# Kernel optimization log

Measured on AMD Instinct MI355X. Metric: run time of the kernel, lower is better.

Reference implementation:

```python
import math
import jax, jax.numpy as jnp
import numpy as np

B, L, D = 8, 4096, 512
FACTOR = 5


def setup_inputs() -> dict:
    key = jax.random.key(0)
    kq, kk, kv = jax.random.split(key, 3)
    q = jax.random.normal(kq, (B, L, D), dtype=jnp.float32)
    k = jax.random.normal(kk, (B, L, D), dtype=jnp.float32)
    v = jax.random.normal(kv, (B, L, D), dtype=jnp.float32)
    return {"q": q, "k": k, "v": v}


def reference(q, k, v):
    # ProbSparse attention (sparse=True branch, L_Q > 1)
    L_Q = q.shape[1]
    scale = q.shape[-1] ** -0.5
    # scores: [B, L_Q, L_K]
    scores = jnp.einsum('bqd,bkd->bqk', q, k) * scale
    # sparsity measure M = max - mean over keys: [B, L_Q]
    M = scores.max(axis=-1) - scores.mean(axis=-1)
    u = max(1, int(FACTOR * math.log(L_Q + 1)))
    u = min(u, L_Q)  # static python int (u = 41 here)
    _, top_idx = jax.lax.top_k(M, u)  # [B, u]
    # gather top-u query rows of scores, softmax over keys (row-wise softmax
    # commutes with row selection, so this matches softmax-then-gather)
    scores_top = jnp.take_along_axis(scores, top_idx[:, :, None], axis=1)  # [B, u, L_K]
    attn = jax.nn.softmax(scores_top, axis=-1)
    out_top = jnp.einsum('buk,bkd->bud', attn, v)  # [B, u, D]
    # non-selected queries receive the mean value
    v_mean = jnp.broadcast_to(v.mean(axis=1, keepdims=True), v.shape)  # [B, L, D]
    b_idx = jnp.arange(q.shape[0])[:, None]  # [B, 1]
    out = v_mean.at[b_idx, top_idx].set(out_top)
    return out
```

## Files before the change

### kernel.cpp

```cpp
#include <hip/hip_runtime.h>
#include <math.h>

#define B_ 8
#define L_ 4096
#define D_ 512
#define U_ 41
#define NSL 32

static constexpr float SCALE = 0.044194173824159216f;

typedef __attribute__((ext_vector_type(8))) short bf16x8;
typedef __attribute__((ext_vector_type(4))) float f32x4;
typedef unsigned int uint;


__global__ __launch_bounds__(512) void kSumsV4(const float* __restrict__ k,
                                               const float* __restrict__ v,
                                               float* __restrict__ partk,
                                               float* __restrict__ partv) {
  const int s = blockIdx.x;
  const int b = blockIdx.y;
  const int rg = threadIdx.x >> 7;
  const int dc = threadIdx.x & 127;
  const int row0 = s * 128 + rg * 32;
  const float* kp = k + ((size_t)(b * L_ + row0)) * D_ + dc * 4;
  const float* vp = v + ((size_t)(b * L_ + row0)) * D_ + dc * 4;
  float4 ks = make_float4(0.f, 0.f, 0.f, 0.f);
  float4 vs = make_float4(0.f, 0.f, 0.f, 0.f);
  for (int l = 0; l < 32; ++l) {
    float4 t = *(const float4*)(kp + (size_t)l * D_);
    float4 u = *(const float4*)(vp + (size_t)l * D_);
    ks.x += t.x; ks.y += t.y; ks.z += t.z; ks.w += t.w;
    vs.x += u.x; vs.y += u.y; vs.z += u.z; vs.w += u.w;
  }
  const int p = (b * NSL + s) * 4 + rg;
  *(float4*)(partk + (size_t)p * D_ + dc * 4) = ks;
  *(float4*)(partv + (size_t)p * D_ + dc * 4) = vs;
}

__global__ __launch_bounds__(512) void kSums2V(const float* __restrict__ partk,
                                               const float* __restrict__ partv,
                                               float* __restrict__ ksum,
                                               float* __restrict__ vmean) {
  const int b = blockIdx.x;
  const int d = threadIdx.x;
  float ks = 0.f, vs = 0.f;
  for (int p = 0; p < 128; ++p) {
    ks += partk[((size_t)(b * 128 + p)) * D_ + d];
    vs += partv[((size_t)(b * 128 + p)) * D_ + d];
  }
  ksum[b * D_ + d] = ks;
  vmean[b * D_ + d] = vs * (1.f / L_);
}

__global__ __launch_bounds__(512) void kSums1(const float* __restrict__ k,
                                              const float* __restrict__ v,
                                              float* __restrict__ partk,
                                              float* __restrict__ partv) {
  const int s = blockIdx.x;
  const int b = blockIdx.y;
  const int d = threadIdx.x;
  const int rows = L_ / NSL;
  const size_t base = ((size_t)b * L_ + (size_t)s * rows) * D_ + d;
  float ks = 0.f, vs = 0.f;
  for (int l = 0; l < rows; ++l) {
    ks += k[base + (size_t)l * D_];
    vs += v[base + (size_t)l * D_];
  }
  partk[(b * NSL + s) * D_ + d] = ks;
  partv[(b * NSL + s) * D_ + d] = vs;
}

__global__ __launch_bounds__(512) void kSums2(const float* __restrict__ partk,
                                              const float* __restrict__ partv,
                                              float* __restrict__ ksum,
                                              float* __restrict__ vmean) {
  const int b = blockIdx.x;
  const int d = threadIdx.x;
  float ks = 0.f, vs = 0.f;
  for (int s = 0; s < NSL; ++s) {
    ks += partk[(b * NSL + s) * D_ + d];
    vs += partv[(b * NSL + s) * D_ + d];
  }
  ksum[b * D_ + d] = ks;
  vmean[b * D_ + d] = vs * (1.f / L_);
}

__global__ __launch_bounds__(256) void kMeanM(const float* __restrict__ q,
                                              const float* __restrict__ ksum,
                                              const float* __restrict__ pmax,
                                              float* __restrict__ M) {
  __shared__ float ks[D_];
  const int gid = blockIdx.x * 256 + threadIdx.x;
  const int b = gid >> 12;
  for (int i = threadIdx.x; i < D_; i += 256) ks[i] = ksum[b * D_ + i];
  __syncthreads();
  const float* qp = q + (size_t)gid * D_;
  float acc = 0.f;
  for (int i = 0; i < D_; i += 4) {
    float4 t = *(const float4*)(qp + i);
    acc += t.x * ks[i] + t.y * ks[i + 1] + t.z * ks[i + 2] + t.w * ks[i + 3];
  }
  const float rowmax = fmaxf(pmax[gid], pmax[B_ * L_ + gid]);
  M[gid] = SCALE * (rowmax - acc * (1.f / L_));
}

__global__ __launch_bounds__(256) void kTopK3(const float* __restrict__ M,
                                              int* __restrict__ topidx) {
  __shared__ float wv[2][4];
  __shared__ int wi[2][4];
  const int b = blockIdx.x;
  const int tid = threadIdx.x;
  const int wave = tid >> 6, lane = tid & 63;
  float v[16];
#pragma unroll
  for (int j = 0; j < 16; ++j) v[j] = M[b * L_ + tid + j * 256];
  float bv = v[0];
  int bj = 0;
#pragma unroll
  for (int j = 1; j < 16; ++j)
    if (v[j] > bv) { bv = v[j]; bj = j; }
  int bi = tid + bj * 256;

  for (int it = 0; it < U_; ++it) {
    float rv = bv;
    int ri = bi;
#pragma unroll
    for (int off = 1; off < 64; off <<= 1) {
      float ov = __shfl_xor(rv, off);
      int oi = __shfl_xor(ri, off);
      if (ov > rv || (ov == rv && oi < ri)) { rv = ov; ri = oi; }
    }
    const int par = it & 1;
    if (lane == 0) { wv[par][wave] = rv; wi[par][wave] = ri; }
    __syncthreads();
    float gv = wv[par][0];
    int gi = wi[par][0];
#pragma unroll
    for (int w = 1; w < 4; ++w) {
      float ov = wv[par][w];
      int oi = wi[par][w];
      if (ov > gv || (ov == gv && oi < gi)) { gv = ov; gi = oi; }
    }
    if (tid == 0) topidx[b * U_ + it] = gi;
    if (gi == bi) {
      const int jb = gi >> 8;
#pragma unroll
      for (int j = 0; j < 16; ++j)
        if (j == jb) v[j] = -3.4e38f;
      bv = v[0];
      bj = 0;
#pragma unroll
      for (int j = 1; j < 16; ++j)
        if (v[j] > bv) { bv = v[j]; bj = j; }
      bi = tid + bj * 256;
    }
  }
}

__global__ __launch_bounds__(64) void kTopK4(const float* __restrict__ pmax,
                                             const float* __restrict__ qdot,
                                             int* __restrict__ topidx) {
  const int b = blockIdx.x;
  const int lane = threadIdx.x;
  float v[64];
#pragma unroll
  for (int j = 0; j < 64; ++j) {
    const int gid = b * L_ + lane + j * 64;
    v[j] = SCALE * (fmaxf(pmax[gid], pmax[B_ * L_ + gid]) - qdot[gid] * (1.f / L_));
  }
  float bv = v[0];
  int bj = 0;
#pragma unroll
  for (int j = 1; j < 64; ++j)
    if (v[j] > bv) { bv = v[j]; bj = j; }
  int bi = lane + bj * 64;

  for (int it = 0; it < U_; ++it) {
    float rv = bv;
    int ri = bi;
#pragma unroll
    for (int off = 1; off < 64; off <<= 1) {
      float ov = __shfl_xor(rv, off);
      int oi = __shfl_xor(ri, off);
      if (ov > rv || (ov == rv && oi < ri)) { rv = ov; ri = oi; }
    }
    if (lane == 0) topidx[b * U_ + it] = ri;
    if (ri == bi) {
#pragma unroll
      for (int j = 0; j < 64; ++j)
        if (j == bj) v[j] = -3.4e38f;
      bv = v[0];
      bj = 0;
#pragma unroll
      for (int j = 1; j < 64; ++j)
        if (v[j] > bv) { bv = v[j]; bj = j; }
      bi = lane + bj * 64;
    }
  }
}

__global__ __launch_bounds__(256) void kFill(const float* __restrict__ vmean,
                                             float* __restrict__ out) {
  const int g = blockIdx.x * 256 + threadIdx.x;
  const int d4 = g & 127;
  const int bl = g >> 7;
  const int b = bl >> 12;
  ((float4*)out)[g] = ((const float4*)vmean)[b * 128 + d4];
}

__device__ inline uint bf16_rne_bits(float x) {
  uint u = __builtin_bit_cast(uint, x);
  return (u + 0x7FFFu + ((u >> 16) & 1u)) >> 16;
}
__device__ inline float bits_to_f32(uint hi16) {
  return __builtin_bit_cast(float, hi16 << 16);
}

__global__ __launch_bounds__(256) void kConvert(const float* __restrict__ src,
                                                unsigned char* __restrict__ dhi,
                                                unsigned char* __restrict__ dlo) {
  const int cid = blockIdx.x * 256 + threadIdx.x;
  const int c16 = cid & 7;
  const int row = (cid >> 3) & 127;
  const int dsi = (cid >> 10) & 7;
  const int rt = (cid >> 13) & 31;
  const int b = cid >> 18;
  const int l = rt * 128 + row;
  const int d = dsi * 64 + c16 * 8;
  const float* sp = src + ((size_t)(b * L_ + l) * D_ + d);
  float x[8];
  *(float4*)(x) = *(const float4*)sp;
  *(float4*)(x + 4) = *(const float4*)(sp + 4);
  uint hw[4], lw[4];
#pragma unroll
  for (int p = 0; p < 4; ++p) {
    float a = x[2 * p], c = x[2 * p + 1];
    uint ha = bf16_rne_bits(a), hc = bf16_rne_bits(c);
    float ra = a - bits_to_f32(ha);
    float rc = c - bits_to_f32(hc);
    uint la = bf16_rne_bits(ra), lc = bf16_rne_bits(rc);
    hw[p] = ha | (hc << 16);
    lw[p] = la | (lc << 16);
  }
  const size_t dstByte = ((size_t)(cid >> 3) << 7) +
                         (uint)((c16 << 4) ^ ((row & 7) << 4));
  *(uint4*)(dhi + dstByte) = make_uint4(hw[0], hw[1], hw[2], hw[3]);
  *(uint4*)(dlo + dstByte) = make_uint4(lw[0], lw[1], lw[2], lw[3]);
}

__global__ __launch_bounds__(256) void kConvertQdot(const float* __restrict__ src,
                                                    const float* __restrict__ ksum,
                                                    unsigned char* __restrict__ dhi,
                                                    unsigned char* __restrict__ dlo,
                                                    float* __restrict__ qdotp) {
  const int cid = blockIdx.x * 256 + threadIdx.x;
  const int c16 = cid & 7;
  const int row = (cid >> 3) & 127;
  const int dsi = (cid >> 10) & 7;
  const int rt = (cid >> 13) & 31;
  const int b = cid >> 18;
  const int l = rt * 128 + row;
  const int d = dsi * 64 + c16 * 8;
  const float* sp = src + ((size_t)(b * L_ + l) * D_ + d);
  float x[8];
  *(float4*)(x) = *(const float4*)sp;
  *(float4*)(x + 4) = *(const float4*)(sp + 4);

  const float* kp = ksum + b * D_ + d;
  float dot = 0.f;
#pragma unroll
  for (int i = 0; i < 8; ++i) dot += x[i] * kp[i];
#pragma unroll
  for (int off = 1; off < 8; off <<= 1) dot += __shfl_xor(dot, off);

  uint hw[4], lw[4];
#pragma unroll
  for (int p = 0; p < 4; ++p) {
    float a = x[2 * p], c = x[2 * p + 1];
    uint ha = bf16_rne_bits(a), hc = bf16_rne_bits(c);
    float ra = a - bits_to_f32(ha);
    float rc = c - bits_to_f32(hc);
    uint la = bf16_rne_bits(ra), lc = bf16_rne_bits(rc);
    hw[p] = ha | (hc << 16);
    lw[p] = la | (lc << 16);
  }
  const size_t dstByte = ((size_t)(cid >> 3) << 7) +
                         (uint)((c16 << 4) ^ ((row & 7) << 4));
  *(uint4*)(dhi + dstByte) = make_uint4(hw[0], hw[1], hw[2], hw[3]);
  *(uint4*)(dlo + dstByte) = make_uint4(lw[0], lw[1], lw[2], lw[3]);
  if (c16 == 0)
    qdotp[((size_t)dsi * B_ * L_) + b * L_ + l] = dot;
}

__global__ __launch_bounds__(256) void kQdotReduce(const float* __restrict__ qdotp,
                                                   float* __restrict__ qdot) {
  const int gid = blockIdx.x * 256 + threadIdx.x;
  float s = 0.f;
#pragma unroll
  for (int i = 0; i < 8; ++i) s += qdotp[(size_t)i * B_ * L_ + gid];
  qdot[gid] = s;
}

__device__ __forceinline__ void gload16(const unsigned char* g, unsigned char* l) {
  __builtin_amdgcn_global_load_lds(
      (const __attribute__((address_space(1))) unsigned int*)(g),
      (__attribute__((address_space(3))) unsigned int*)(l), 16, 0, 0);
}

__global__ __launch_bounds__(256, 2) void kRowMaxB(const unsigned char* __restrict__ qhi,
                                                   const unsigned char* __restrict__ qlo,
                                                   const unsigned char* __restrict__ khi,
                                                   const unsigned char* __restrict__ klo,
                                                   float* __restrict__ pmax) {
  __shared__ unsigned char lds[65536];
  __shared__ float red[256];
  unsigned char* ldsQhi = lds;
  unsigned char* ldsQlo = lds + 16384;
  unsigned char* ldsKhi = lds + 32768;
  unsigned char* ldsKlo = lds + 49152;

  const int b = blockIdx.y;
  const int qt = blockIdx.x;
  const int kh = blockIdx.z;
  const int tid = threadIdx.x;
  const int lane = tid & 63;
  const int wave = tid >> 6;
  const int wq = wave >> 1, wk = wave & 1;

  const size_t qtb = ((size_t)((b * 32 + qt) * 8)) * 16384;
  const unsigned char* qhB = qhi + qtb;
  const unsigned char* qlB = qlo + qtb;

  float rmax[4][4];
#pragma unroll
  for (int i = 0; i < 4; ++i)
#pragma unroll
    for (int j = 0; j < 4; ++j) rmax[i][j] = -3.4e38f;

  for (int kt = 0; kt < 16; ++kt) {
    const size_t ktb = ((size_t)((b * 32 + (kh * 16 + kt)) * 8)) * 16384;
    const unsigned char* khB = khi + ktb;
    const unsigned char* klB = klo + ktb;

    f32x4 acc[4][4];
#pragma unroll
    for (int i = 0; i < 4; ++i)
#pragma unroll
      for (int j = 0; j < 4; ++j)
#pragma unroll
        for (int e = 0; e < 4; ++e) acc[i][j][e] = 0.f;

    for (int dsi = 0; dsi < 8; ++dsi) {
      __syncthreads();
      {
        const size_t dof = (size_t)dsi * 16384 + (size_t)tid * 16;
        const size_t lof = (size_t)tid * 16;
#pragma unroll
        for (int i = 0; i < 4; ++i) {
          gload16(qhB + dof + i * 4096, ldsQhi + lof + i * 4096);
          gload16(qlB + dof + i * 4096, ldsQlo + lof + i * 4096);
          gload16(khB + dof + i * 4096, ldsKhi + lof + i * 4096);
          gload16(klB + dof + i * 4096, ldsKlo + lof + i * 4096);
        }
      }
      __syncthreads();

#pragma unroll
      for (int h = 0; h < 2; ++h) {
        const int rbyte = h * 64 + ((lane >> 4) << 4);
        bf16x8 aH[4], aL[4], bH[4], bL[4];
#pragma unroll
        for (int f = 0; f < 4; ++f) {
          const int qrow = wq * 64 + f * 16 + (lane & 15);
          const int krow = wk * 64 + f * 16 + (lane & 15);
          const int qoff = qrow * 128 + (rbyte ^ ((qrow & 7) << 4));
          const int koff = krow * 128 + (rbyte ^ ((krow & 7) << 4));
          aH[f] = *(const bf16x8*)(ldsQhi + qoff);
          aL[f] = *(const bf16x8*)(ldsQlo + qoff);
          bH[f] = *(const bf16x8*)(ldsKhi + koff);
          bL[f] = *(const bf16x8*)(ldsKlo + koff);
        }
#pragma unroll
        for (int mf = 0; mf < 4; ++mf)
#pragma unroll
          for (int nf = 0; nf < 4; ++nf) {
            acc[mf][nf] = __builtin_amdgcn_mfma_f32_16x16x32_bf16(aH[mf], bH[nf], acc[mf][nf], 0, 0, 0);
            acc[mf][nf] = __builtin_amdgcn_mfma_f32_16x16x32_bf16(aH[mf], bL[nf], acc[mf][nf], 0, 0, 0);
            acc[mf][nf] = __builtin_amdgcn_mfma_f32_16x16x32_bf16(aL[mf], bH[nf], acc[mf][nf], 0, 0, 0);
          }
      }
    }
#pragma unroll
    for (int mf = 0; mf < 4; ++mf)
#pragma unroll
      for (int r = 0; r < 4; ++r) {
        float m = fmaxf(fmaxf(acc[mf][0][r], acc[mf][1][r]),
                        fmaxf(acc[mf][2][r], acc[mf][3][r]));
        rmax[mf][r] = fmaxf(rmax[mf][r], m);
      }
  }

#pragma unroll
  for (int mf = 0; mf < 4; ++mf)
#pragma unroll
    for (int r = 0; r < 4; ++r) {
      float v = rmax[mf][r];
#pragma unroll
      for (int off = 1; off < 16; off <<= 1) v = fmaxf(v, __shfl_xor(v, off));
      rmax[mf][r] = v;
    }

  if ((lane & 15) == 0) {
#pragma unroll
    for (int mf = 0; mf < 4; ++mf)
#pragma unroll
      for (int r = 0; r < 4; ++r) {
        const int rowl = wq * 64 + mf * 16 + ((lane >> 4) << 2) + r;
        red[wk * 128 + rowl] = rmax[mf][r];
      }
  }
  __syncthreads();
  if (tid < 128) {
    pmax[(size_t)kh * B_ * L_ + (size_t)b * L_ + qt * 128 + tid] =
        fmaxf(red[tid], red[128 + tid]);
  }
}


__global__ __launch_bounds__(64) void kGatherQ(const float* __restrict__ q,
                                               const int* __restrict__ topidx,
                                               unsigned char* __restrict__ qselhi,
                                               unsigned char* __restrict__ qsello) {
  const int j = blockIdx.x;
  const int b = blockIdx.y;
  const int lane = threadIdx.x;
  const int dsi = lane >> 3;
  const int c16 = lane & 7;
  float x[8] = {0.f, 0.f, 0.f, 0.f, 0.f, 0.f, 0.f, 0.f};
  if (j < U_) {
    const int row = topidx[b * U_ + j];
    const float* sp = q + ((size_t)(b * L_ + row)) * D_ + dsi * 64 + c16 * 8;
    *(float4*)(x) = *(const float4*)sp;
    *(float4*)(x + 4) = *(const float4*)(sp + 4);
  }
  uint hw[4], lw[4];
#pragma unroll
  for (int p = 0; p < 4; ++p) {
    float a = x[2 * p], c = x[2 * p + 1];
    uint ha = bf16_rne_bits(a), hc = bf16_rne_bits(c);
    float ra = a - bits_to_f32(ha);
    float rc = c - bits_to_f32(hc);
    uint la = bf16_rne_bits(ra), lc = bf16_rne_bits(rc);
    hw[p] = ha | (hc << 16);
    lw[p] = la | (lc << 16);
  }
  const size_t dstByte = ((size_t)((b * 8 + dsi) * 64 + j)) * 128 +
                         (uint)((c16 << 4) ^ ((j & 7) << 4));
  *(uint4*)(qselhi + dstByte) = make_uint4(hw[0], hw[1], hw[2], hw[3]);
  *(uint4*)(qsello + dstByte) = make_uint4(lw[0], lw[1], lw[2], lw[3]);
}

__global__ __launch_bounds__(256) void kSelScoresM(const unsigned char* __restrict__ qselhi,
                                                   const unsigned char* __restrict__ qsello,
                                                   const unsigned char* __restrict__ khi,
                                                   const unsigned char* __restrict__ klo,
                                                   float* __restrict__ P) {
  __shared__ unsigned char lds[49152];
  unsigned char* ldsQhi = lds;
  unsigned char* ldsQlo = lds + 8192;
  unsigned char* ldsKhi = lds + 16384;
  unsigned char* ldsKlo = lds + 32768;

  const int kc = blockIdx.x;
  const int b = blockIdx.y;
  const int tid = threadIdx.x;
  const int lane = tid & 63;
  const int wave = tid >> 6;
  const int wq = wave >> 1, wk = wave & 1;

  const size_t ktb = ((size_t)((b * 32 + kc) * 8)) * 16384;
  const unsigned char* khB = khi + ktb;
  const unsigned char* klB = klo + ktb;
  const size_t qb = ((size_t)b * 8) * 8192;
  const unsigned char* qhB = qselhi + qb;
  const unsigned char* qlB = qsello + qb;

  f32x4 acc[2][4];
#pragma unroll
  for (int i = 0; i < 2; ++i)
#pragma unroll
    for (int j = 0; j < 4; ++j)
#pragma unroll
      for (int e = 0; e < 4; ++e) acc[i][j][e] = 0.f;

  for (int dsi = 0; dsi < 8; ++dsi) {
    __syncthreads();
    {
      const size_t qof = (size_t)dsi * 8192 + (size_t)tid * 16;
      const size_t kof = (size_t)dsi * 16384 + (size_t)tid * 16;
      const size_t lof = (size_t)tid * 16;
#pragma unroll
      for (int i = 0; i < 2; ++i) {
        gload16(qhB + qof + i * 4096, ldsQhi + lof + i * 4096);
        gload16(qlB + qof + i * 4096, ldsQlo + lof + i * 4096);
      }
#pragma unroll
      for (int i = 0; i < 4; ++i) {
        gload16(khB + kof + i * 4096, ldsKhi + lof + i * 4096);
        gload16(klB + kof + i * 4096, ldsKlo + lof + i * 4096);
      }
    }
    __syncthreads();

#pragma unroll
    for (int h = 0; h < 2; ++h) {
      const int rbyte = h * 64 + ((lane >> 4) << 4);
      bf16x8 aH[2], aL[2], bH[4], bL[4];
#pragma unroll
      for (int f = 0; f < 2; ++f) {
        const int qrow = wq * 32 + f * 16 + (lane & 15);
        const int qoff = qrow * 128 + (rbyte ^ ((qrow & 7) << 4));
        aH[f] = *(const bf16x8*)(ldsQhi + qoff);
        aL[f] = *(const bf16x8*)(ldsQlo + qoff);
      }
#pragma unroll
      for (int f = 0; f < 4; ++f) {
        const int krow = wk * 64 + f * 16 + (lane & 15);
        const int koff = krow * 128 + (rbyte ^ ((krow & 7) << 4));
        bH[f] = *(const bf16x8*)(ldsKhi + koff);
        bL[f] = *(const bf16x8*)(ldsKlo + koff);
      }
#pragma unroll
      for (int mf = 0; mf < 2; ++mf)
#pragma unroll
        for (int nf = 0; nf < 4; ++nf) {
          acc[mf][nf] = __builtin_amdgcn_mfma_f32_16x16x32_bf16(aH[mf], bH[nf], acc[mf][nf], 0, 0, 0);
          acc[mf][nf] = __builtin_amdgcn_mfma_f32_16x16x32_bf16(aH[mf], bL[nf], acc[mf][nf], 0, 0, 0);
          acc[mf][nf] = __builtin_amdgcn_mfma_f32_16x16x32_bf16(aL[mf], bH[nf], acc[mf][nf], 0, 0, 0);
        }
    }
  }

#pragma unroll
  for (int mf = 0; mf < 2; ++mf)
#pragma unroll
    for (int nf = 0; nf < 4; ++nf)
#pragma unroll
      for (int r = 0; r < 4; ++r) {
        const int row = wq * 32 + mf * 16 + ((lane >> 4) << 2) + r;
        const int key = kc * 128 + wk * 64 + nf * 16 + (lane & 15);
        if (row < U_)
          P[((size_t)(b * U_ + row)) * L_ + key] = acc[mf][nf][r];
      }
}

__global__ __launch_bounds__(256) void kSoftmaxP(float* __restrict__ P) {
  __shared__ float red[256];
  const int j = blockIdx.x, b = blockIdx.y;
  float* row = P + ((size_t)(b * U_ + j)) * L_;
  const int tid = threadIdx.x;
  float v[16];
  float mx = -3.4e38f;
#pragma unroll
  for (int i = 0; i < 16; ++i) {
    v[i] = row[tid + i * 256];
    mx = fmaxf(mx, v[i]);
  }
  red[tid] = mx;
  __syncthreads();
  for (int s = 128; s > 0; s >>= 1) {
    if (tid < s) red[tid] = fmaxf(red[tid], red[tid + s]);
    __syncthreads();
  }
  mx = red[0];
  __syncthreads();
  float sum = 0.f;
#pragma unroll
  for (int i = 0; i < 16; ++i) {
    float e = expf((v[i] - mx) * SCALE);
    v[i] = e;
    sum += e;
  }
  red[tid] = sum;
  __syncthreads();
  for (int s = 128; s > 0; s >>= 1) {
    if (tid < s) red[tid] += red[tid + s];
    __syncthreads();
  }
  const float inv = 1.f / red[0];
#pragma unroll
  for (int i = 0; i < 16; ++i) row[tid + i * 256] = v[i] * inv;
}

__global__ __launch_bounds__(256) void kPV(const float* __restrict__ P,
                                           const float* __restrict__ v,
                                           float* __restrict__ partial) {
  __shared__ float plds[41 * 128];
  const int kc = blockIdx.x;
  const int dc = blockIdx.y;
  const int b = blockIdx.z;
  const int tid = threadIdx.x;
  const int trow = tid >> 7, dcol = tid & 127;
  float acc[U_];
#pragma unroll
  for (int j = 0; j < U_; ++j) acc[j] = 0.f;

  for (int sub = 0; sub < 4; ++sub) {
    const int key0 = kc * 512 + sub * 128;
    __syncthreads();
    for (int idx = tid; idx < U_ * 128; idx += 256)
      plds[idx] = P[((size_t)(b * U_ + (idx >> 7))) * L_ + key0 + (idx & 127)];
    __syncthreads();
    const float* vp = v + ((size_t)(b * L_ + key0 + trow * 64)) * D_ + dc * 128 + dcol;
    float vv[64];
#pragma unroll
    for (int kk = 0; kk < 64; ++kk) vv[kk] = vp[(size_t)kk * D_];
#pragma unroll
    for (int j = 0; j < U_; ++j) {
      const float4* pr = (const float4*)&plds[j * 128 + trow * 64];
      float a = acc[j];
#pragma unroll
      for (int q4 = 0; q4 < 16; ++q4) {
        float4 p4 = pr[q4];
        a = fmaf(p4.x, vv[q4 * 4 + 0], a);
        a = fmaf(p4.y, vv[q4 * 4 + 1], a);
        a = fmaf(p4.z, vv[q4 * 4 + 2], a);
        a = fmaf(p4.w, vv[q4 * 4 + 3], a);
      }
      acc[j] = a;
    }
  }
  float* pp = partial + ((size_t)((b * 4 + dc) * 16 + kc * 2 + trow)) * (U_ * 128) + dcol;
#pragma unroll
  for (int j = 0; j < U_; ++j) pp[j * 128] = acc[j];
}

__global__ __launch_bounds__(256) void kPVout(const float* __restrict__ partial,
                                              const int* __restrict__ topidx,
                                              float* __restrict__ out) {
  const int j = blockIdx.x, b = blockIdx.y;
  const int tid = threadIdx.x;
  const int l = topidx[b * U_ + j];
#pragma unroll
  for (int h = 0; h < 2; ++h) {
    const int d = tid + h * 256;
    const int dc = d >> 7, dcol = d & 127;
    float s = 0.f;
#pragma unroll
    for (int part = 0; part < 16; ++part)
      s += partial[((size_t)((b * 4 + dc) * 16 + part)) * (U_ * 128) + j * 128 + dcol];
    out[((size_t)(b * L_ + l)) * D_ + d] = s;
  }
}


__device__ inline void stageHalfRow(const float* __restrict__ src,
                                    char* hiBase, char* loBase,
                                    int row, int shalf) {
  const int sw = (row & 7) << 4;
  char* hp = hiBase + row * 128;
  char* lp = loBase + row * 128;
#pragma unroll
  for (int g = 0; g < 4; ++g) {
    f32x4 x0 = *(const f32x4*)(src + g * 8);
    f32x4 x1 = *(const f32x4*)(src + g * 8 + 4);
    float x[8] = {x0.x, x0.y, x0.z, x0.w, x1.x, x1.y, x1.z, x1.w};
    uint hw[4], lw[4];
#pragma unroll
    for (int p = 0; p < 4; ++p) {
      float a = x[2 * p], c = x[2 * p + 1];
      uint ha = bf16_rne_bits(a), hc = bf16_rne_bits(c);
      float ra = a - bits_to_f32(ha);
      float rc = c - bits_to_f32(hc);
      uint la = bf16_rne_bits(ra), lc = bf16_rne_bits(rc);
      hw[p] = ha | (hc << 16);
      lw[p] = la | (lc << 16);
    }
    const int off = (shalf * 64 + g * 16) ^ sw;
    *(uint4*)(hp + off) = make_uint4(hw[0], hw[1], hw[2], hw[3]);
    *(uint4*)(lp + off) = make_uint4(lw[0], lw[1], lw[2], lw[3]);
  }
}

__global__ __launch_bounds__(256, 2) void kRowMaxM(const float* __restrict__ q,
                                                   const float* __restrict__ k,
                                                   float* __restrict__ pmax) {
  __shared__ char lds[65536];
  __shared__ float red[256];
  char* ldsQhi = lds;
  char* ldsQlo = lds + 16384;
  char* ldsKhi = lds + 32768;
  char* ldsKlo = lds + 49152;

  const int b = blockIdx.y;
  const int qbase = blockIdx.x * 128;
  const int kh = blockIdx.z;
  const int tid = threadIdx.x;
  const int lane = tid & 63;
  const int wave = tid >> 6;
  const int wq = wave >> 1, wk = wave & 1;
  const int srow = tid >> 1;
  const int shalf = tid & 1;

  const float* qrow_base = q + ((size_t)b * L_ + qbase + srow) * D_ + shalf * 32;
  const float* krow_base = k + ((size_t)b * L_ + kh * 2048 + srow) * D_ + shalf * 32;

  float rmax[4][4];
#pragma unroll
  for (int i = 0; i < 4; ++i)
#pragma unroll
    for (int j = 0; j < 4; ++j) rmax[i][j] = -3.4e38f;

  for (int kt = 0; kt < 16; ++kt) {
    f32x4 acc[4][4];
#pragma unroll
    for (int i = 0; i < 4; ++i)
#pragma unroll
      for (int j = 0; j < 4; ++j)
#pragma unroll
        for (int e = 0; e < 4; ++e) acc[i][j][e] = 0.f;

    for (int dsi = 0; dsi < 8; ++dsi) {
      __syncthreads();
      stageHalfRow(qrow_base + dsi * 64, ldsQhi, ldsQlo, srow, shalf);
      stageHalfRow(krow_base + (size_t)kt * 128 * D_ + dsi * 64, ldsKhi, ldsKlo, srow, shalf);
      __syncthreads();

#pragma unroll
      for (int h = 0; h < 2; ++h) {
        const int rbyte = h * 64 + ((lane >> 4) << 4);
        bf16x8 aH[4], aL[4], bH[4], bL[4];
#pragma unroll
        for (int f = 0; f < 4; ++f) {
          const int qrow = wq * 64 + f * 16 + (lane & 15);
          const int krow = wk * 64 + f * 16 + (lane & 15);
          const int qoff = qrow * 128 + (rbyte ^ ((qrow & 7) << 4));
          const int koff = krow * 128 + (rbyte ^ ((krow & 7) << 4));
          aH[f] = *(const bf16x8*)(ldsQhi + qoff);
          aL[f] = *(const bf16x8*)(ldsQlo + qoff);
          bH[f] = *(const bf16x8*)(ldsKhi + koff);
          bL[f] = *(const bf16x8*)(ldsKlo + koff);
        }
#pragma unroll
        for (int mf = 0; mf < 4; ++mf)
#pragma unroll
          for (int nf = 0; nf < 4; ++nf) {
            acc[mf][nf] = __builtin_amdgcn_mfma_f32_16x16x32_bf16(aH[mf], bH[nf], acc[mf][nf], 0, 0, 0);
            acc[mf][nf] = __builtin_amdgcn_mfma_f32_16x16x32_bf16(aH[mf], bL[nf], acc[mf][nf], 0, 0, 0);
            acc[mf][nf] = __builtin_amdgcn_mfma_f32_16x16x32_bf16(aL[mf], bH[nf], acc[mf][nf], 0, 0, 0);
          }
      }
    }
#pragma unroll
    for (int mf = 0; mf < 4; ++mf)
#pragma unroll
      for (int r = 0; r < 4; ++r) {
        float m = fmaxf(fmaxf(acc[mf][0][r], acc[mf][1][r]),
                        fmaxf(acc[mf][2][r], acc[mf][3][r]));
        rmax[mf][r] = fmaxf(rmax[mf][r], m);
      }
  }

#pragma unroll
  for (int mf = 0; mf < 4; ++mf)
#pragma unroll
    for (int r = 0; r < 4; ++r) {
      float v = rmax[mf][r];
#pragma unroll
      for (int off = 1; off < 16; off <<= 1) v = fmaxf(v, __shfl_xor(v, off));
      rmax[mf][r] = v;
    }

  if ((lane & 15) == 0) {
#pragma unroll
    for (int mf = 0; mf < 4; ++mf)
#pragma unroll
      for (int r = 0; r < 4; ++r) {
        const int rowl = wq * 64 + mf * 16 + ((lane >> 4) << 2) + r;
        red[wk * 128 + rowl] = rmax[mf][r];
      }
  }
  __syncthreads();
  if (tid < 128) {
    pmax[(size_t)kh * B_ * L_ + (size_t)b * L_ + qbase + tid] =
        fmaxf(red[tid], red[128 + tid]);
  }
}

__global__ __launch_bounds__(256) void kAttnSel(const float* __restrict__ q,
                                                const float* __restrict__ k,
                                                const float* __restrict__ v,
                                                const int* __restrict__ topidx,
                                                float* __restrict__ out) {
  __shared__ float qs[D_];
  __shared__ float sc[L_];
  __shared__ float wred[4];
  __shared__ float sred[256];
  const int b = blockIdx.y;
  const int l_sel = topidx[b * U_ + blockIdx.x];
  const int tid = threadIdx.x;
  const int wave = tid >> 6, lane = tid & 63;
  const float* qrow = q + ((size_t)b * L_ + l_sel) * D_;
  qs[tid] = qrow[tid];
  qs[tid + 256] = qrow[tid + 256];
  __syncthreads();
  float qr[8];
#pragma unroll
  for (int i = 0; i < 8; ++i) qr[i] = qs[lane * 8 + i];
  float wmax = -3.4e38f;
  for (int l = wave; l < L_; l += 4) {
    const float* kp = k + ((size_t)b * L_ + l) * D_ + lane * 8;
    float4 k0 = *(const float4*)kp;
    float4 k1 = *(const float4*)(kp + 4);
    float p = k0.x * qr[0] + k0.y * qr[1] + k0.z * qr[2] + k0.w * qr[3] +
              k1.x * qr[4] + k1.y * qr[5] + k1.z * qr[6] + k1.w * qr[7];
#pragma unroll
    for (int off = 32; off > 0; off >>= 1) p += __shfl_xor(p, off);
    if (lane == 0) sc[l] = p;
    wmax = fmaxf(wmax, p);
  }
  if (lane == 0) wred[wave] = wmax;
  __syncthreads();
  const float mx = fmaxf(fmaxf(wred[0], wred[1]), fmaxf(wred[2], wred[3]));
  float psum = 0.f;
  for (int i = tid; i < L_; i += 256) {
    float e = expf((sc[i] - mx) * SCALE);
    sc[i] = e;
    psum += e;
  }
  sred[tid] = psum;
  __syncthreads();
  for (int s = 128; s > 0; s >>= 1) {
    if (tid < s) sred[tid] += sred[tid + s];
    __syncthreads();
  }
  const float inv = 1.f / sred[0];
  float a0a = 0.f, a0b = 0.f, a1a = 0.f, a1b = 0.f;
  const float* vb = v + (size_t)b * L_ * D_;
  for (int l = 0; l < L_; l += 2) {
    float p0 = sc[l], p1 = sc[l + 1];
    const float* vp0 = vb + (size_t)l * D_;
    const float* vp1 = vp0 + D_;
    a0a = fmaf(p0, vp0[tid], a0a);
    a1a = fmaf(p0, vp0[tid + 256], a1a);
    a0b = fmaf(p1, vp1[tid], a0b);
    a1b = fmaf(p1, vp1[tid + 256], a1b);
  }
  float* orow = out + ((size_t)b * L_ + l_sel) * D_;
  orow[tid] = (a0a + a0b) * inv;
  orow[tid + 256] = (a1a + a1b) * inv;
}


extern "C" void kernel_launch(void* const* d_in, const int* in_sizes, int n_in,
                              void* d_out, int out_size, void* d_ws, size_t ws_size,
                              hipStream_t stream) {
  const float* q = (const float*)d_in[0];
  const float* k = (const float*)d_in[1];
  const float* v = (const float*)d_in[2];
  float* out = (float*)d_out;
  unsigned char* wsb = (unsigned char*)d_ws;

  const size_t NEED = 71731200;

  if (ws_size >= NEED) {
    unsigned char* qhiW = wsb;
    unsigned char* qloW = wsb + 33554432;
    float* P = (float*)wsb;
    float* partial = (float*)(wsb + 5373952);
    unsigned char* qselhi = wsb + 16121856;
    unsigned char* qsello = wsb + 16646144;
    float* pmax = (float*)(wsb + 67108864);
    float* qdot = (float*)(wsb + 67371008);
    float* ksum = (float*)(wsb + 67502080);
    float* vmean = (float*)(wsb + 67518464);
    int* tidx = (int*)(wsb + 67534848);
    float* partk = (float*)(wsb + 67536896);
    float* partv = (float*)(wsb + 69634048);
    float* qdotp = partk;

    unsigned char* khiO = (unsigned char*)d_out;
    unsigned char* kloO = khiO + 33554432;

    kSumsV4<<<dim3(NSL, B_), 512, 0, stream>>>(k, v, partk, partv);
    kSums2V<<<B_, 512, 0, stream>>>(partk, partv, ksum, vmean);
    kConvertQdot<<<8192, 256, 0, stream>>>(q, ksum, qhiW, qloW, qdotp);
    kQdotReduce<<<B_ * L_ / 256, 256, 0, stream>>>(qdotp, qdot);
    kConvert<<<8192, 256, 0, stream>>>(k, khiO, kloO);
    kRowMaxB<<<dim3(32, B_, 2), 256, 0, stream>>>(qhiW, qloW, khiO, kloO, pmax);
    kTopK4<<<B_, 64, 0, stream>>>(pmax, qdot, tidx);
    kGatherQ<<<dim3(64, B_), 64, 0, stream>>>(q, tidx, qselhi, qsello);
    kSelScoresM<<<dim3(32, B_), 256, 0, stream>>>(qselhi, qsello, khiO, kloO, P);
    kSoftmaxP<<<dim3(U_, B_), 256, 0, stream>>>(P);
    kFill<<<B_ * L_ * D_ / 1024, 256, 0, stream>>>(vmean, out);
    kPV<<<dim3(8, 4, B_), 256, 0, stream>>>(P, v, partial);
    kPVout<<<dim3(U_, B_), 256, 0, stream>>>(partial, tidx, out);
  } else {
    float* ws = (float*)d_ws;
    float* Marr = ws;
    float* pmax = ws + 32768;
    float* ksum = ws + 98304;
    float* vmean = ws + 102400;
    int* tidx = (int*)(ws + 106496);
    float* partk = ws + 107008;
    float* partv = ws + 107008 + B_ * NSL * D_;

    kSums1<<<dim3(NSL, B_), 512, 0, stream>>>(k, v, partk, partv);
    kSums2<<<B_, 512, 0, stream>>>(partk, partv, ksum, vmean);
    kRowMaxM<<<dim3(L_ / 128, B_, 2), 256, 0, stream>>>(q, k, pmax);
    kMeanM<<<B_ * L_ / 256, 256, 0, stream>>>(q, ksum, pmax, Marr);
    kTopK3<<<B_, 256, 0, stream>>>(Marr, tidx);
    kFill<<<B_ * L_ * D_ / 1024, 256, 0, stream>>>(vmean, out);
    kAttnSel<<<dim3(U_, B_), 256, 0, stream>>>(q, k, v, tidx, out);
  }
}
```

Before: 601.3 us.

## Double-buffer row-max GEMM with 32-wide d-slices and flattened k-loop

The bf16 hi/lo split layout goes from 64-column to 32-column d-slices with a matching 4-chunk XOR swizzle. The converter, gather and selected-scores kernels, and the qdot reduce (now 16 partials), are all updated to the new layout. The row-max kernel now runs one flattened loop over 256 stages with two 32 KB LDS buffers. The next stage's global-to-LDS loads are issued before the current stage's MFMAs, hiding load latency and dropping one barrier per step, at the cost of smaller per-stage MFMA work.

```diff
diff --git a/kernel.cpp b/kernel.cpp
--- a/kernel.cpp
+++ b/kernel.cpp
@@ -221,13 +221,13 @@
                                                 unsigned char* __restrict__ dhi,
                                                 unsigned char* __restrict__ dlo) {
   const int cid = blockIdx.x * 256 + threadIdx.x;
-  const int c16 = cid & 7;
-  const int row = (cid >> 3) & 127;
-  const int dsi = (cid >> 10) & 7;
+  const int c = cid & 3;
+  const int row = (cid >> 2) & 127;
+  const int dsi = (cid >> 9) & 15;
   const int rt = (cid >> 13) & 31;
   const int b = cid >> 18;
   const int l = rt * 128 + row;
-  const int d = dsi * 64 + c16 * 8;
+  const int d = dsi * 32 + c * 8;
   const float* sp = src + ((size_t)(b * L_ + l) * D_ + d);
   float x[8];
   *(float4*)(x) = *(const float4*)sp;
@@ -235,16 +235,16 @@
   uint hw[4], lw[4];
 #pragma unroll
   for (int p = 0; p < 4; ++p) {
-    float a = x[2 * p], c = x[2 * p + 1];
-    uint ha = bf16_rne_bits(a), hc = bf16_rne_bits(c);
+    float a = x[2 * p], cc = x[2 * p + 1];
+    uint ha = bf16_rne_bits(a), hc = bf16_rne_bits(cc);
     float ra = a - bits_to_f32(ha);
-    float rc = c - bits_to_f32(hc);
+    float rc = cc - bits_to_f32(hc);
     uint la = bf16_rne_bits(ra), lc = bf16_rne_bits(rc);
     hw[p] = ha | (hc << 16);
     lw[p] = la | (lc << 16);
   }
-  const size_t dstByte = ((size_t)(cid >> 3) << 7) +
-                         (uint)((c16 << 4) ^ ((row & 7) << 4));
+  const size_t dstByte = ((size_t)(cid >> 2) << 6) +
+                         (uint)((c ^ ((row >> 1) & 3)) << 4);
   *(uint4*)(dhi + dstByte) = make_uint4(hw[0], hw[1], hw[2], hw[3]);
   *(uint4*)(dlo + dstByte) = make_uint4(lw[0], lw[1], lw[2], lw[3]);
 }
@@ -255,13 +255,13 @@
                                                     unsigned char* __restrict__ dlo,
                                                     float* __restrict__ qdotp) {
   const int cid = blockIdx.x * 256 + threadIdx.x;
-  const int c16 = cid & 7;
-  const int row = (cid >> 3) & 127;
-  const int dsi = (cid >> 10) & 7;
+  const int c = cid & 3;
+  const int row = (cid >> 2) & 127;
+  const int dsi = (cid >> 9) & 15;
   const int rt = (cid >> 13) & 31;
   const int b = cid >> 18;
   const int l = rt * 128 + row;
-  const int d = dsi * 64 + c16 * 8;
+  const int d = dsi * 32 + c * 8;
   const float* sp = src + ((size_t)(b * L_ + l) * D_ + d);
   float x[8];
   *(float4*)(x) = *(const float4*)sp;
@@ -271,25 +271,25 @@
   float dot = 0.f;
 #pragma unroll
   for (int i = 0; i < 8; ++i) dot += x[i] * kp[i];
-#pragma unroll
-  for (int off = 1; off < 8; off <<= 1) dot += __shfl_xor(dot, off);
+  dot += __shfl_xor(dot, 1);
+  dot += __shfl_xor(dot, 2);
 
   uint hw[4], lw[4];
 #pragma unroll
   for (int p = 0; p < 4; ++p) {
-    float a = x[2 * p], c = x[2 * p + 1];
-    uint ha = bf16_rne_bits(a), hc = bf16_rne_bits(c);
+    float a = x[2 * p], cc = x[2 * p + 1];
+    uint ha = bf16_rne_bits(a), hc = bf16_rne_bits(cc);
     float ra = a - bits_to_f32(ha);
-    float rc = c - bits_to_f32(hc);
+    float rc = cc - bits_to_f32(hc);
     uint la = bf16_rne_bits(ra), lc = bf16_rne_bits(rc);
     hw[p] = ha | (hc << 16);
     lw[p] = la | (lc << 16);
   }
-  const size_t dstByte = ((size_t)(cid >> 3) << 7) +
-                         (uint)((c16 << 4) ^ ((row & 7) << 4));
+  const size_t dstByte = ((size_t)(cid >> 2) << 6) +
+                         (uint)((c ^ ((row >> 1) & 3)) << 4);
   *(uint4*)(dhi + dstByte) = make_uint4(hw[0], hw[1], hw[2], hw[3]);
   *(uint4*)(dlo + dstByte) = make_uint4(lw[0], lw[1], lw[2], lw[3]);
-  if (c16 == 0)
+  if (c == 0)
     qdotp[((size_t)dsi * B_ * L_) + b * L_ + l] = dot;
 }
 
@@ -298,7 +298,7 @@
   const int gid = blockIdx.x * 256 + threadIdx.x;
   float s = 0.f;
 #pragma unroll
-  for (int i = 0; i < 8; ++i) s += qdotp[(size_t)i * B_ * L_ + gid];
+  for (int i = 0; i < 16; ++i) s += qdotp[(size_t)i * B_ * L_ + gid];
   qdot[gid] = s;
 }
 
@@ -308,17 +308,15 @@
       (__attribute__((address_space(3))) unsigned int*)(l), 16, 0, 0);
 }
 
-__global__ __launch_bounds__(256, 2) void kRowMaxB(const unsigned char* __restrict__ qhi,
+__global__ __launch_bounds__(256, 2) void kRowMaxD(const unsigned char* __restrict__ qhi,
                                                    const unsigned char* __restrict__ qlo,
                                                    const unsigned char* __restrict__ khi,
                                                    const unsigned char* __restrict__ klo,
                                                    float* __restrict__ pmax) {
   __shared__ unsigned char lds[65536];
   __shared__ float red[256];
-  unsigned char* ldsQhi = lds;
-  unsigned char* ldsQlo = lds + 16384;
-  unsigned char* ldsKhi = lds + 32768;
-  unsigned char* ldsKlo = lds + 49152;
+  unsigned char* buf0 = lds;
+  unsigned char* buf1 = lds + 32768;
 
   const int b = blockIdx.y;
   const int qt = blockIdx.x;
@@ -327,78 +325,86 @@
   const int lane = tid & 63;
   const int wave = tid >> 6;
   const int wq = wave >> 1, wk = wave & 1;
-
-  const size_t qtb = ((size_t)((b * 32 + qt) * 8)) * 16384;
-  const unsigned char* qhB = qhi + qtb;
-  const unsigned char* qlB = qlo + qtb;
+  const int g4 = lane >> 4;
+
+  const unsigned char* qhB = qhi + (size_t)(b * 32 + qt) * 131072;
+  const unsigned char* qlB = qlo + (size_t)(b * 32 + qt) * 131072;
+  const unsigned char* khB = khi + (size_t)(b * 32 + kh * 16) * 131072;
+  const unsigned char* klB = klo + (size_t)(b * 32 + kh * 16) * 131072;
+
+  const size_t lof = (size_t)tid * 16;
+
+  auto STAGE = [&](int s, unsigned char* buf) {
+    const int kt = s >> 4, dsi = s & 15;
+    const size_t qof = (size_t)dsi * 8192 + lof;
+    const size_t kof = (size_t)kt * 131072 + (size_t)dsi * 8192 + lof;
+    gload16(qhB + qof, buf + lof);
+    gload16(qhB + qof + 4096, buf + lof + 4096);
+    gload16(qlB + qof, buf + 8192 + lof);
+    gload16(qlB + qof + 4096, buf + 8192 + lof + 4096);
+    gload16(khB + kof, buf + 16384 + lof);
+    gload16(khB + kof + 4096, buf + 16384 + lof + 4096);
+    gload16(klB + kof, buf + 24576 + lof);
+    gload16(klB + kof + 4096, buf + 24576 + lof + 4096);
+  };
 
   float rmax[4][4];
+  f32x4 acc[4][4];
 #pragma unroll
   for (int i = 0; i < 4; ++i)
 #pragma unroll
-    for (int j = 0; j < 4; ++j) rmax[i][j] = -3.4e38f;
-
-  for (int kt = 0; kt < 16; ++kt) {
-    const size_t ktb = ((size_t)((b * 32 + (kh * 16 + kt)) * 8)) * 16384;
-    const unsigned char* khB = khi + ktb;
-    const unsigned char* klB = klo + ktb;
-
-    f32x4 acc[4][4];
-#pragma unroll
-    for (int i = 0; i < 4; ++i)
-#pragma unroll
-      for (int j = 0; j < 4; ++j)
-#pragma unroll
-        for (int e = 0; e < 4; ++e) acc[i][j][e] = 0.f;
-
-    for (int dsi = 0; dsi < 8; ++dsi) {
-      __syncthreads();
-      {
-        const size_t dof = (size_t)dsi * 16384 + (size_t)tid * 16;
-        const size_t lof = (size_t)tid * 16;
-#pragma unroll
-        for (int i = 0; i < 4; ++i) {
-          gload16(qhB + dof + i * 4096, ldsQhi + lof + i * 4096);
-          gload16(qlB + dof + i * 4096, ldsQlo + lof + i * 4096);
-          gload16(khB + dof + i * 4096, ldsKhi + lof + i * 4096);
-          gload16(klB + dof + i * 4096, ldsKlo + lof + i * 4096);
+    for (int j = 0; j < 4; ++j) {
+      rmax[i][j] = -3.4e38f;
+#pragma unroll
+      for (int e = 0; e < 4; ++e) acc[i][j][e] = 0.f;
+    }
+
+  int qaddr[4], kaddr[4];
+#pragma unroll
+  for (int f = 0; f < 4; ++f) {
+    const int qrow = wq * 64 + f * 16 + (lane & 15);
+    const int krow = wk * 64 + f * 16 + (lane & 15);
+    qaddr[f] = qrow * 64 + ((g4 ^ ((qrow >> 1) & 3)) << 4);
+    kaddr[f] = krow * 64 + ((g4 ^ ((krow >> 1) & 3)) << 4);
+  }
+
+  auto PHASE = [&](int s, const unsigned char* bufR, unsigned char* bufW) {
+    __syncthreads();
+    if (s < 255) STAGE(s + 1, bufW);
+    bf16x8 aH[4], aL[4], bH[4], bL[4];
+#pragma unroll
+    for (int f = 0; f < 4; ++f) {
+      aH[f] = *(const bf16x8*)(bufR + qaddr[f]);
+      aL[f] = *(const bf16x8*)(bufR + 8192 + qaddr[f]);
+      bH[f] = *(const bf16x8*)(bufR + 16384 + kaddr[f]);
+      bL[f] = *(const bf16x8*)(bufR + 24576 + kaddr[f]);
+    }
+#pragma unroll
+    for (int mf = 0; mf < 4; ++mf)
+#pragma unroll
+      for (int nf = 0; nf < 4; ++nf) {
+        acc[mf][nf] = __builtin_amdgcn_mfma_f32_16x16x32_bf16(aH[mf], bH[nf], acc[mf][nf], 0, 0, 0);
+        acc[mf][nf] = __builtin_amdgcn_mfma_f32_16x16x32_bf16(aH[mf], bL[nf], acc[mf][nf], 0, 0, 0);
+        acc[mf][nf] = __builtin_amdgcn_mfma_f32_16x16x32_bf16(aL[mf], bH[nf], acc[mf][nf], 0, 0, 0);
+      }
+    if ((s & 15) == 15) {
+#pragma unroll
+      for (int mf = 0; mf < 4; ++mf)
+#pragma unroll
+        for (int r = 0; r < 4; ++r) {
+          float m = fmaxf(fmaxf(acc[mf][0][r], acc[mf][1][r]),
+                          fmaxf(acc[mf][2][r], acc[mf][3][r]));
+          rmax[mf][r] = fmaxf(rmax[mf][r], m);
+#pragma unroll
+          for (int nf = 0; nf < 4; ++nf) acc[mf][nf][r] = 0.f;
         }
-      }
-      __syncthreads();
-
-#pragma unroll
-      for (int h = 0; h < 2; ++h) {
-        const int rbyte = h * 64 + ((lane >> 4) << 4);
-        bf16x8 aH[4], aL[4], bH[4], bL[4];
-#pragma unroll
-        for (int f = 0; f < 4; ++f) {
-          const int qrow = wq * 64 + f * 16 + (lane & 15);
-          const int krow = wk * 64 + f * 16 + (lane & 15);
-          const int qoff = qrow * 128 + (rbyte ^ ((qrow & 7) << 4));
-          const int koff = krow * 128 + (rbyte ^ ((krow & 7) << 4));
-          aH[f] = *(const bf16x8*)(ldsQhi + qoff);
-          aL[f] = *(const bf16x8*)(ldsQlo + qoff);
-          bH[f] = *(const bf16x8*)(ldsKhi + koff);
-          bL[f] = *(const bf16x8*)(ldsKlo + koff);
-        }
-#pragma unroll
-        for (int mf = 0; mf < 4; ++mf)
-#pragma unroll
-          for (int nf = 0; nf < 4; ++nf) {
-            acc[mf][nf] = __builtin_amdgcn_mfma_f32_16x16x32_bf16(aH[mf], bH[nf], acc[mf][nf], 0, 0, 0);
-            acc[mf][nf] = __builtin_amdgcn_mfma_f32_16x16x32_bf16(aH[mf], bL[nf], acc[mf][nf], 0, 0, 0);
-            acc[mf][nf] = __builtin_amdgcn_mfma_f32_16x16x32_bf16(aL[mf], bH[nf], acc[mf][nf], 0, 0, 0);
-          }
-      }
-    }
-#pragma unroll
-    for (int mf = 0; mf < 4; ++mf)
-#pragma unroll
-      for (int r = 0; r < 4; ++r) {
-        float m = fmaxf(fmaxf(acc[mf][0][r], acc[mf][1][r]),
-                        fmaxf(acc[mf][2][r], acc[mf][3][r]));
-        rmax[mf][r] = fmaxf(rmax[mf][r], m);
-      }
+    }
+  };
+
+  STAGE(0, buf0);
+  for (int s = 0; s < 256; s += 2) {
+    PHASE(s, buf0, buf1);
+    PHASE(s + 1, buf1, buf0);
   }
 
 #pragma unroll
@@ -435,28 +441,28 @@
   const int j = blockIdx.x;
   const int b = blockIdx.y;
   const int lane = threadIdx.x;
-  const int dsi = lane >> 3;
-  const int c16 = lane & 7;
+  const int dsi = lane >> 2;
+  const int c = lane & 3;
   float x[8] = {0.f, 0.f, 0.f, 0.f, 0.f, 0.f, 0.f, 0.f};
   if (j < U_) {
     const int row = topidx[b * U_ + j];
-    const float* sp = q + ((size_t)(b * L_ + row)) * D_ + dsi * 64 + c16 * 8;
+    const float* sp = q + ((size_t)(b * L_ + row)) * D_ + dsi * 32 + c * 8;
     *(float4*)(x) = *(const float4*)sp;
     *(float4*)(x + 4) = *(const float4*)(sp + 4);
   }
   uint hw[4], lw[4];
 #pragma unroll
   for (int p = 0; p < 4; ++p) {
-    float a = x[2 * p], c = x[2 * p + 1];
-    uint ha = bf16_rne_bits(a), hc = bf16_rne_bits(c);
+    float a = x[2 * p], cc = x[2 * p + 1];
+    uint ha = bf16_rne_bits(a), hc = bf16_rne_bits(cc);
     float ra = a - bits_to_f32(ha);
-    float rc = c - bits_to_f32(hc);
+    float rc = cc - bits_to_f32(hc);
     uint la = bf16_rne_bits(ra), lc = bf16_rne_bits(rc);
     hw[p] = ha | (hc << 16);
     lw[p] = la | (lc << 16);
   }
-  const size_t dstByte = ((size_t)((b * 8 + dsi) * 64 + j)) * 128 +
-                         (uint)((c16 << 4) ^ ((j & 7) << 4));
+  const size_t dstByte = (size_t)((b * 16 + dsi) * 64 + j) * 64 +
+                         (uint)((c ^ ((j >> 1) & 3)) << 4);
   *(uint4*)(qselhi + dstByte) = make_uint4(hw[0], hw[1], hw[2], hw[3]);
   *(uint4*)(qsello + dstByte) = make_uint4(lw[0], lw[1], lw[2], lw[3]);
 }
@@ -466,25 +472,31 @@
                                                    const unsigned char* __restrict__ khi,
                                                    const unsigned char* __restrict__ klo,
                                                    float* __restrict__ P) {
-  __shared__ unsigned char lds[49152];
-  unsigned char* ldsQhi = lds;
-  unsigned char* ldsQlo = lds + 8192;
-  unsigned char* ldsKhi = lds + 16384;
-  unsigned char* ldsKlo = lds + 32768;
-
+  __shared__ unsigned char lds[24576];
   const int kc = blockIdx.x;
   const int b = blockIdx.y;
   const int tid = threadIdx.x;
   const int lane = tid & 63;
   const int wave = tid >> 6;
   const int wq = wave >> 1, wk = wave & 1;
-
-  const size_t ktb = ((size_t)((b * 32 + kc) * 8)) * 16384;
-  const unsigned char* khB = khi + ktb;
-  const unsigned char* klB = klo + ktb;
-  const size_t qb = ((size_t)b * 8) * 8192;
-  const unsigned char* qhB = qselhi + qb;
-  const unsigned char* qlB = qsello + qb;
+  const int g4 = lane >> 4;
+
+  const unsigned char* khB = khi + (size_t)(b * 32 + kc) * 131072;
+  const unsigned char* klB = klo + (size_t)(b * 32 + kc) * 131072;
+  const unsigned char* qhB = qselhi + (size_t)b * 65536;
+  const unsigned char* qlB = qsello + (size_t)b * 65536;
+
+  int qaddr[2], kaddr[4];
+#pragma unroll
+  for (int f = 0; f < 2; ++f) {
+    const int qrow = wq * 32 + f * 16 + (lane & 15);
+    qaddr[f] = qrow * 64 + ((g4 ^ ((qrow >> 1) & 3)) << 4);
+  }
+#pragma unroll
+  for (int f = 0; f < 4; ++f) {
+    const int krow = wk * 64 + f * 16 + (lane & 15);
+    kaddr[f] = krow * 64 + ((g4 ^ ((krow >> 1) & 3)) << 4);
+  }
 
   f32x4 acc[2][4];
 #pragma unroll
@@ -494,52 +506,40 @@
 #pragma unroll
       for (int e = 0; e < 4; ++e) acc[i][j][e] = 0.f;
 
-  for (int dsi = 0; dsi < 8; ++dsi) {
+  const size_t lof = (size_t)tid * 16;
+  for (int dsi = 0; dsi < 16; ++dsi) {
     __syncthreads();
     {
-      const size_t qof = (size_t)dsi * 8192 + (size_t)tid * 16;
-      const size_t kof = (size_t)dsi * 16384 + (size_t)tid * 16;
-      const size_t lof = (size_t)tid * 16;
-#pragma unroll
-      for (int i = 0; i < 2; ++i) {
-        gload16(qhB + qof + i * 4096, ldsQhi + lof + i * 4096);
-        gload16(qlB + qof + i * 4096, ldsQlo + lof + i * 4096);
+      const size_t qof = (size_t)dsi * 4096 + lof;
+      const size_t kof = (size_t)dsi * 8192 + lof;
+      gload16(qhB + qof, lds + lof);
+      gload16(qlB + qof, lds + 4096 + lof);
+      gload16(khB + kof, lds + 8192 + lof);
+      gload16(khB + kof + 4096, lds + 8192 + lof + 4096);
+      gload16(klB + kof, lds + 16384 + lof);
+      gload16(klB + kof + 4096, lds + 16384 + lof + 4096);
+    }
+    __syncthreads();
+
+    bf16x8 aH[2], aL[2], bH[4], bL[4];
+#pragma unroll
+    for (int f = 0; f < 2; ++f) {
+      aH[f] = *(const bf16x8*)(lds + qaddr[f]);
+      aL[f] = *(const bf16x8*)(lds + 4096 + qaddr[f]);
+    }
+#pragma unroll
+    for (int f = 0; f < 4; ++f) {
+      bH[f] = *(const bf16x8*)(lds + 8192 + kaddr[f]);
+      bL[f] = *(const bf16x8*)(lds + 16384 + kaddr[f]);
+    }
+#pragma unroll
+    for (int mf = 0; mf < 2; ++mf)
+#pragma unroll
+      for (int nf = 0; nf < 4; ++nf) {
+        acc[mf][nf] = __builtin_amdgcn_mfma_f32_16x16x32_bf16(aH[mf], bH[nf], acc[mf][nf], 0, 0, 0);
+        acc[mf][nf] = __builtin_amdgcn_mfma_f32_16x16x32_bf16(aH[mf], bL[nf], acc[mf][nf], 0, 0, 0);
+        acc[mf][nf] = __builtin_amdgcn_mfma_f32_16x16x32_bf16(aL[mf], bH[nf], acc[mf][nf], 0, 0, 0);
       }
-#pragma unroll
-      for (int i = 0; i < 4; ++i) {
-        gload16(khB + kof + i * 4096, ldsKhi + lof + i * 4096);
-        gload16(klB + kof + i * 4096, ldsKlo + lof + i * 4096);
-      }
-    }
-    __syncthreads();
-
-#pragma unroll
-    for (int h = 0; h < 2; ++h) {
-      const int rbyte = h * 64 + ((lane >> 4) << 4);
-      bf16x8 aH[2], aL[2], bH[4], bL[4];
-#pragma unroll
-      for (int f = 0; f < 2; ++f) {
-        const int qrow = wq * 32 + f * 16 + (lane & 15);
-        const int qoff = qrow * 128 + (rbyte ^ ((qrow & 7) << 4));
-        aH[f] = *(const bf16x8*)(ldsQhi + qoff);
-        aL[f] = *(const bf16x8*)(ldsQlo + qoff);
-      }
-#pragma unroll
-      for (int f = 0; f < 4; ++f) {
-        const int krow = wk * 64 + f * 16 + (lane & 15);
-        const int koff = krow * 128 + (rbyte ^ ((krow & 7) << 4));
-        bH[f] = *(const bf16x8*)(ldsKhi + koff);
-        bL[f] = *(const bf16x8*)(ldsKlo + koff);
-      }
-#pragma unroll
-      for (int mf = 0; mf < 2; ++mf)
-#pragma unroll
-        for (int nf = 0; nf < 4; ++nf) {
-          acc[mf][nf] = __builtin_amdgcn_mfma_f32_16x16x32_bf16(aH[mf], bH[nf], acc[mf][nf], 0, 0, 0);
-          acc[mf][nf] = __builtin_amdgcn_mfma_f32_16x16x32_bf16(aH[mf], bL[nf], acc[mf][nf], 0, 0, 0);
-          acc[mf][nf] = __builtin_amdgcn_mfma_f32_16x16x32_bf16(aL[mf], bH[nf], acc[mf][nf], 0, 0, 0);
-        }
-    }
   }
 
 #pragma unroll
@@ -888,7 +888,7 @@
     kConvertQdot<<<8192, 256, 0, stream>>>(q, ksum, qhiW, qloW, qdotp);
     kQdotReduce<<<B_ * L_ / 256, 256, 0, stream>>>(qdotp, qdot);
     kConvert<<<8192, 256, 0, stream>>>(k, khiO, kloO);
-    kRowMaxB<<<dim3(32, B_, 2), 256, 0, stream>>>(qhiW, qloW, khiO, kloO, pmax);
+    kRowMaxD<<<dim3(32, B_, 2), 256, 0, stream>>>(qhiW, qloW, khiO, kloO, pmax);
     kTopK4<<<B_, 64, 0, stream>>>(pmax, qdot, tidx);
     kGatherQ<<<dim3(64, B_), 64, 0, stream>>>(q, tidx, qselhi, qsello);
     kSelScoresM<<<dim3(32, B_), 256, 0, stream>>>(qselhi, qsello, khiO, kloO, P);
```

New measurement: 652.7 us. +8.6%, slower.
